# Kernel optimization log

Measured on AMD Instinct MI355X. Metric: run time of the kernel, lower is better.

## Reference

```python
import jax, jax.numpy as jnp
import numpy as np

HEAD_DIM = 64  # self.head_dim, used only as the attention scale
D_MODEL = 1024


def setup_inputs() -> dict:
    key = jax.random.key(0)
    ks = jax.random.split(key, 6)
    B, S_NEW, S_CACHE, D = 4, 2048, 6144, D_MODEL
    w_scale = 1.0 / np.sqrt(D)  # keep logits well-conditioned
    return {
        "hidden_states": jax.random.normal(ks[0], (B, S_NEW, D), dtype=jnp.float32),
        "cached_key": jax.random.normal(ks[1], (B, S_CACHE, D), dtype=jnp.float32),
        "cached_value": jax.random.normal(ks[2], (B, S_CACHE, D), dtype=jnp.float32),
        "Wq": jax.random.normal(ks[3], (D, D), dtype=jnp.float32) * w_scale,
        "bq": jnp.zeros((D,), dtype=jnp.float32),
        "Wk": jax.random.normal(ks[4], (D, D), dtype=jnp.float32) * w_scale,
        "bk": jnp.zeros((D,), dtype=jnp.float32),
        "Wv": jax.random.normal(ks[5], (D, D), dtype=jnp.float32) * w_scale,
        "bv": jnp.zeros((D,), dtype=jnp.float32),
    }


def reference(hidden_states, cached_key, cached_value, Wq, bq, Wk, bk, Wv, bv):
    # Cached-branch forward: project new K/V, append to cache, full attention.
    # torch.nn.Linear: x @ W.T + b
    q = jnp.einsum("bsd,ed->bse", hidden_states, Wq) + bq          # [B, Sq, D]
    new_k = jnp.einsum("bsd,ed->bse", hidden_states, Wk) + bk      # [B, Sq, D]
    new_v = jnp.einsum("bsd,ed->bse", hidden_states, Wv) + bv
    k = jnp.concatenate([cached_key, new_k], axis=1)               # [B, Skv, D]
    v = jnp.concatenate([cached_value, new_v], axis=1)
    scale = 1.0 / jnp.sqrt(jnp.asarray(HEAD_DIM, dtype=q.dtype))
    scores = jnp.einsum("bqd,bkd->bqk", q, k) * scale              # [B, Sq, Skv]
    probs = jax.nn.softmax(scores, axis=-1)
    out = jnp.einsum("bqk,bkd->bqd", probs, v)                     # [B, Sq, D]
    return out
```

## Files before the change

### kernel.cpp

```cpp
#include <hip/hip_runtime.h>
#include <stdint.h>


#define DM 1024
#define NB 4
#define SQN 2048
#define SCC 6144
#define SKV 8192
#define NSPLIT 2
#define KSP (SKV / NSPLIT)

typedef unsigned short u16;
typedef __attribute__((ext_vector_type(8))) short short8;
typedef __attribute__((ext_vector_type(4))) float f32x4;

__device__ __forceinline__ u16 f2bf(float x) {
  unsigned u = __builtin_bit_cast(unsigned, x);
  u += 0x7fffu + ((u >> 16) & 1u);
  return (u16)(u >> 16);
}

__device__ __forceinline__ void gll16(const void* g, void* l) {
  __builtin_amdgcn_global_load_lds(
      (const __attribute__((address_space(1))) void*)g,
      (__attribute__((address_space(3))) void*)l, 16, 0, 0);
}

#define FENCE() asm volatile("" ::: "memory")
#define BARRIER()                      \
  do {                                 \
    FENCE();                           \
    __builtin_amdgcn_s_barrier();      \
    FENCE();                           \
  } while (0)

__global__ __launch_bounds__(256) void k_cvt(const float* __restrict__ in,
                                             u16* __restrict__ out, long n4) {
  long i = (long)blockIdx.x * 256 + threadIdx.x;
  long st = (long)gridDim.x * 256;
  for (; i < n4; i += st) {
    float4 v = ((const float4*)in)[i];
    ushort4 u;
    u.x = f2bf(v.x); u.y = f2bf(v.y); u.z = f2bf(v.z); u.w = f2bf(v.w);
    ((ushort4*)out)[i] = u;
  }
}

__global__ __launch_bounds__(256) void k_cvt_ck(const float* __restrict__ in,
                                                u16* __restrict__ out) {
  const long n4 = (long)NB * SCC * DM / 4;
  long i = (long)blockIdx.x * 256 + threadIdx.x;
  long st = (long)gridDim.x * 256;
  for (; i < n4; i += st) {
    float4 v = ((const float4*)in)[i];
    ushort4 u;
    u.x = f2bf(v.x); u.y = f2bf(v.y); u.z = f2bf(v.z); u.w = f2bf(v.w);
    long e = i * 4;
    int b = (int)(e / ((long)SCC * DM));
    long rem = e - (long)b * SCC * DM;
    *(ushort4*)(out + (long)b * SKV * DM + rem) = u;
  }
}

__global__ __launch_bounds__(256) void k_build_vt(const float* __restrict__ cv,
                                                  const u16* __restrict__ vtmp,
                                                  u16* __restrict__ VT) {
  __shared__ u16 t[64][65];
  const int kv0 = blockIdx.x * 64;
  const int d0 = blockIdx.y * 64;
  const int b = blockIdx.z;
  const int c = threadIdx.x & 63;
  const int r4 = threadIdx.x >> 6;
#pragma unroll
  for (int p = 0; p < 16; ++p) {
    int kr = p * 4 + r4;
    int kv = kv0 + kr;
    int d = d0 + c;
    u16 u;
    if (kv < SCC)
      u = f2bf(cv[((long)b * SCC + kv) * DM + d]);
    else
      u = vtmp[((long)b * SQN + (kv - SCC)) * DM + d];
    t[kr][c] = u;
  }
  __syncthreads();
#pragma unroll
  for (int p = 0; p < 16; ++p) {
    int dr = p * 4 + r4;
    VT[((long)b * DM + d0 + dr) * SKV + kv0 + c] = t[c][dr];
  }
}

template <int MODE>
__global__ __launch_bounds__(512, 2) void k_gemm8(
    const u16* __restrict__ A, const u16* __restrict__ B0,
    void* __restrict__ C0, void* __restrict__ C1, void* __restrict__ C2,
    float* __restrict__ sums, const float* __restrict__ bias0,
    const float* __restrict__ bias1, const float* __restrict__ bias2) {
  extern __shared__ char smem[];
  const int tid = threadIdx.x;
  const int lane = tid & 63;
  const int wv = tid >> 6;
  const int wr = wv >> 2;
  const int wc = wv & 3;
  const int bm = blockIdx.y * 256;
  const int bn = blockIdx.x * 256;
  const int z = blockIdx.z;

  constexpr int LD = (MODE == 2) ? SKV : DM;
  constexpr int NT = ((MODE == 2) ? KSP : DM) / 64;

  const u16 *Ab, *Bb;
  if constexpr (MODE == 0) {
    Ab = A + (long)bm * LD;
    Bb = B0 + (long)bn * LD;
  } else if constexpr (MODE == 1) {
    Ab = A + ((long)z * SKV + bm) * LD;
    Bb = B0 + ((long)z * SQN + bn) * LD;
  } else {
    const int bb_ = z / NSPLIT, sp = z % NSPLIT;
    Ab = A + ((long)bb_ * SQN + bm) * (long)SKV + (long)sp * KSP;
    Bb = B0 + ((long)bb_ * DM + bn) * (long)SKV + (long)sp * KSP;
  }

  const int srow = wv * 8 + (lane >> 3);
  const int scol = ((lane & 7) ^ (lane >> 3)) * 8;
  const u16* gA = Ab + (long)srow * LD + scol;
  const u16* gB = Bb + (long)srow * LD + scol;
  u16* lA = (u16*)smem + wv * 512 + lane * 8;
  u16* lB = (u16*)(smem + 65536) + wv * 512 + lane * 8;

#pragma unroll
  for (int r = 0; r < 4; ++r) gll16(gA + (long)r * 64 * LD, lA + r * 4096);
#pragma unroll
  for (int r = 0; r < 4; ++r) gll16(gB + (long)r * 64 * LD, lB + r * 4096);

  f32x4 acc[8][4];
#pragma unroll
  for (int m = 0; m < 8; ++m)
#pragma unroll
    for (int n = 0; n < 4; ++n)
#pragma unroll
      for (int j = 0; j < 4; ++j) acc[m][n][j] = 0.0f;

  const int alane = lane & 15;
  const int sw = lane & 7;
  const int s0 = lane >> 4;

#define AFRAG(M, KK)                                                  \
  (*(const short8*)(As + (wr * 128 + (M)*16 + alane) * 128 +          \
                    (((s0 + 4 * (KK)) ^ sw) * 16)))
#define BFRAG(N, KK)                                                  \
  (*(const short8*)(Bs + (wc * 64 + (N)*16 + alane) * 128 +           \
                    (((s0 + 4 * (KK)) ^ sw) * 16)))
#define MFMA16(N0, N1)                                                      \
  __builtin_amdgcn_s_setprio(1);                                            \
  _Pragma("unroll") for (int m = 0; m < 8; ++m) {                           \
    acc[m][N0] = __builtin_amdgcn_mfma_f32_16x16x32_bf16(aF[m], bF[N0],     \
                                                         acc[m][N0], 0, 0, 0); \
    acc[m][N1] = __builtin_amdgcn_mfma_f32_16x16x32_bf16(aF[m], bF[N1],     \
                                                         acc[m][N1], 0, 0, 0); \
  }                                                                         \
  __builtin_amdgcn_s_setprio(0);

  short8 aF[8], bF[4];

  for (int kt = 0; kt < NT; ++kt) {
    const int b = kt & 1;
    const char* As = smem + b * 32768;
    const char* Bs = smem + 65536 + b * 32768;
    const int d = (b ^ 1) * 16384;
    const long knext = (long)((kt + 1 < NT) ? kt + 1 : kt) * 64;
    const u16* gAn = gA + knext;
    const u16* gBn = gB + knext;

    gll16(gAn, lA + d);
    gll16(gAn + (long)64 * LD, lA + d + 4096);
    asm volatile("s_waitcnt vmcnt(2)" ::: "memory");
    BARRIER();
#pragma unroll
    for (int m = 0; m < 8; ++m) aF[m] = AFRAG(m, 0);
#pragma unroll
    for (int n = 0; n < 4; ++n) bF[n] = BFRAG(n, 0);
    MFMA16(0, 1);
    BARRIER();

    gll16(gAn + (long)128 * LD, lA + d + 2 * 4096);
    gll16(gAn + (long)192 * LD, lA + d + 3 * 4096);
    BARRIER();
    MFMA16(2, 3);
    BARRIER();

#pragma unroll
    for (int m = 0; m < 8; ++m) aF[m] = AFRAG(m, 1);
#pragma unroll
    for (int n = 0; n < 4; ++n) bF[n] = BFRAG(n, 1);
    gll16(gBn, lB + d);
    gll16(gBn + (long)64 * LD, lB + d + 4096);
    BARRIER();
    MFMA16(0, 1);
    BARRIER();

    gll16(gBn + (long)128 * LD, lB + d + 2 * 4096);
    gll16(gBn + (long)192 * LD, lB + d + 3 * 4096);
    BARRIER();
    MFMA16(2, 3);
    BARRIER();
  }
#undef AFRAG
#undef BFRAG
#undef MFMA16

  const int rsub = (lane >> 4) * 4;

  if constexpr (MODE == 0) {
    const int which = bm >> 10;
    const float* bp = which == 0 ? bias0 : (which == 1 ? bias1 : bias2);
    u16* Cq = (u16*)C0;
    u16* Ck = (u16*)C1;
    u16* Cv = (u16*)C2;
    const int od_base = (bm & 1023) + wr * 128 + rsub;
#pragma unroll
    for (int n = 0; n < 4; ++n) {
      int token = bn + wc * 64 + n * 16 + alane;
      u16* dst;
      if (which == 1) {
        int b = token >> 11, ss = token & 2047;
        dst = Ck + ((long)b * SKV + SCC + ss) * DM;
      } else if (which == 0) {
        dst = Cq + (long)token * DM;
      } else {
        dst = Cv + (long)token * DM;
      }
#pragma unroll
      for (int m = 0; m < 8; ++m) {
        int cc = od_base + m * 16;
        float4 bb = *(const float4*)(bp + cc);
        ushort4 u;
        u.x = f2bf(acc[m][n][0] + bb.x);
        u.y = f2bf(acc[m][n][1] + bb.y);
        u.z = f2bf(acc[m][n][2] + bb.z);
        u.w = f2bf(acc[m][n][3] + bb.w);
        *(ushort4*)(dst + cc) = u;
      }
    }
  } else if constexpr (MODE == 1) {
    u16* Pp = (u16*)C0 + (long)z * SQN * SKV;
    float* sb = sums + z * SQN;
    const float CE = 0.18033688011112042f;
    const int kv_base = bm + wr * 128 + rsub;
#pragma unroll
    for (int n = 0; n < 4; ++n) {
      int q = bn + wc * 64 + n * 16 + alane;
      u16* prow = Pp + (long)q * SKV;
      float part = 0.f;
#pragma unroll
      for (int m = 0; m < 8; ++m) {
        int kv = kv_base + m * 16;
        float e0 = exp2f(acc[m][n][0] * CE);
        float e1 = exp2f(acc[m][n][1] * CE);
        float e2 = exp2f(acc[m][n][2] * CE);
        float e3 = exp2f(acc[m][n][3] * CE);
        part += (e0 + e1) + (e2 + e3);
        ushort4 u;
        u.x = f2bf(e0); u.y = f2bf(e1); u.z = f2bf(e2); u.w = f2bf(e3);
        *(ushort4*)(prow + kv) = u;
      }
      part += __shfl_xor(part, 16);
      part += __shfl_xor(part, 32);
      if ((lane >> 4) == 0) atomicAdd(&sb[q], part);
    }
  } else {
    float* Cp = (float*)C0 + (long)z * SQN * DM;
#pragma unroll
    for (int n = 0; n < 4; ++n) {
      int col = bn + wc * 64 + n * 16 + alane;
#pragma unroll
      for (int m = 0; m < 8; ++m)
#pragma unroll
        for (int j = 0; j < 4; ++j) {
          int row = bm + wr * 128 + m * 16 + rsub + j;
          Cp[(long)row * DM + col] = acc[m][n][j];
        }
    }
  }
}

__global__ __launch_bounds__(256) void k_reduce(const float* __restrict__ Op,
                                                const float* __restrict__ sums,
                                                float* __restrict__ out) {
  const long n4 = (long)NB * SQN * DM / 4;
  long i = (long)blockIdx.x * 256 + threadIdx.x;
  if (i >= n4) return;
  long e = i * 4;
  int b = (int)(e / ((long)SQN * DM));
  long rem = e - (long)b * SQN * DM;
  int row = (int)(rem / DM);
  const long z4 = (long)SQN * DM / 4;
  long i0 = (long)(b * NSPLIT) * z4 + (rem >> 2);
  float4 a0 = ((const float4*)Op)[i0];
  float4 a1 = ((const float4*)Op)[i0 + z4];
  float inv = 1.0f / sums[b * SQN + row];
  float4 r;
  r.x = (a0.x + a1.x) * inv;
  r.y = (a0.y + a1.y) * inv;
  r.z = (a0.z + a1.z) * inv;
  r.w = (a0.w + a1.w) * inv;
  ((float4*)out)[i] = r;
}

extern "C" void kernel_launch(void* const* d_in, const int* in_sizes, int n_in,
                              void* d_out, int out_size, void* d_ws, size_t ws_size,
                              hipStream_t stream) {
  const float* hidden = (const float*)d_in[0];
  const float* ck = (const float*)d_in[1];
  const float* cv = (const float*)d_in[2];
  const float* Wq = (const float*)d_in[3];
  const float* bq = (const float*)d_in[4];
  const float* Wk = (const float*)d_in[5];
  const float* bk = (const float*)d_in[6];
  const float* Wv = (const float*)d_in[7];
  const float* bv = (const float*)d_in[8];
  (void)in_sizes; (void)n_in; (void)out_size; (void)ws_size;

  hipFuncSetAttribute(reinterpret_cast<const void*>(&k_gemm8<0>),
                      hipFuncAttributeMaxDynamicSharedMemorySize, 131072);
  hipFuncSetAttribute(reinterpret_cast<const void*>(&k_gemm8<1>),
                      hipFuncAttributeMaxDynamicSharedMemorySize, 131072);
  hipFuncSetAttribute(reinterpret_cast<const void*>(&k_gemm8<2>),
                      hipFuncAttributeMaxDynamicSharedMemorySize, 131072);

  char* base = (char*)d_ws;
  size_t off = 0;
  auto alloc = [&](size_t bytes) {
    char* p = base + off;
    off = (off + bytes + 255) & ~(size_t)255;
    return p;
  };
  u16* Hb = (u16*)alloc((size_t)NB * SQN * DM * 2);
  u16* Wall = (u16*)alloc((size_t)3 * DM * DM * 2);
  u16* Qb = (u16*)alloc((size_t)NB * SQN * DM * 2);
  u16* Kb = (u16*)alloc((size_t)NB * SKV * DM * 2);
  u16* Vtmp = (u16*)alloc((size_t)NB * SQN * DM * 2);
  float* Opart = (float*)base;
  size_t opart_bytes = (size_t)NB * NSPLIT * SQN * DM * 4;
  if (off < opart_bytes) off = (opart_bytes + 255) & ~(size_t)255;
  u16* VT = (u16*)alloc((size_t)NB * DM * SKV * 2);
  u16* P = (u16*)alloc((size_t)NB * SQN * SKV * 2);
  float* sums = (float*)alloc((size_t)NB * SQN * 4);

  k_cvt<<<2048, 256, 0, stream>>>(hidden, Hb, (long)NB * SQN * DM / 4);
  k_cvt<<<512, 256, 0, stream>>>(Wq, Wall, (long)DM * DM / 4);
  k_cvt<<<512, 256, 0, stream>>>(Wk, Wall + (size_t)DM * DM, (long)DM * DM / 4);
  k_cvt<<<512, 256, 0, stream>>>(Wv, Wall + (size_t)2 * DM * DM, (long)DM * DM / 4);
  k_cvt_ck<<<4096, 256, 0, stream>>>(ck, Kb);

  k_gemm8<0><<<dim3(32, 12, 1), 512, 131072, stream>>>(
      Wall, Hb, Qb, Kb, Vtmp, nullptr, bq, bk, bv);

  k_build_vt<<<dim3(SKV / 64, DM / 64, NB), 256, 0, stream>>>(cv, Vtmp, VT);

  hipMemsetAsync(sums, 0, (size_t)NB * SQN * 4, stream);
  k_gemm8<1><<<dim3(SQN / 256, SKV / 256, NB), 512, 131072, stream>>>(
      Kb, Qb, P, nullptr, nullptr, sums, nullptr, nullptr, nullptr);

  k_gemm8<2><<<dim3(DM / 256, SQN / 256, NB * NSPLIT), 512, 131072, stream>>>(
      P, VT, Opart, nullptr, nullptr, nullptr, nullptr, nullptr, nullptr);

  k_reduce<<<(NB * SQN * DM / 4 + 255) / 256, 256, 0, stream>>>(
      Opart, sums, (float*)d_out);
}
```

Before: 475.9 us.

## Hand-schedule LDS fragment reads with inline asm and partial lgkmcnt waits

Replaces the compiler-generated LDS fragment loads in the GEMM main loop with explicit ds_read_b128 inline asm using immediate offsets. The MFMA work is regrouped into four 4x4 quadrants, and fine-grained lgkmcnt waits plus sched_barriers let LDS reads for later quadrants overlap with MFMAs on earlier ones. The goal is to hide LDS latency and reduce address arithmetic. The cost is more live fragment registers and fragile hand scheduling. The asm reads declare no memory clobber, which could let the compiler move them across barriers.

```diff
diff --git a/kernel.cpp b/kernel.cpp
--- a/kernel.cpp
+++ b/kernel.cpp
@@ -32,6 +32,26 @@
     FENCE();                           \
     __builtin_amdgcn_s_barrier();      \
     FENCE();                           \
+  } while (0)
+
+#define DSR(d, a, I) \
+  asm volatile("ds_read_b128 %0, %1 offset:" #I : "=v"(d) : "v"(a))
+
+#define LGKM(N)                                   \
+  do {                                            \
+    asm volatile("s_waitcnt lgkmcnt(" #N ")");    \
+    __builtin_amdgcn_sched_barrier(0);            \
+  } while (0)
+
+#define MFMAQ(AF, BF, MB)                                                   \
+  do {                                                                      \
+    __builtin_amdgcn_s_setprio(1);                                          \
+    _Pragma("unroll") for (int m = 0; m < 4; ++m)                           \
+        _Pragma("unroll") for (int n = 0; n < 4; ++n) acc[(MB) + m][n] =    \
+        __builtin_amdgcn_mfma_f32_16x16x32_bf16(AF[m], BF[n],               \
+                                                acc[(MB) + m][n], 0, 0, 0); \
+    __builtin_amdgcn_s_setprio(0);                                          \
+    __builtin_amdgcn_sched_barrier(0);                                      \
   } while (0)
 
 __global__ __launch_bounds__(256) void k_cvt(const float* __restrict__ in,
@@ -110,23 +130,23 @@
   constexpr int LD = (MODE == 2) ? SKV : DM;
   constexpr int NT = ((MODE == 2) ? KSP : DM) / 64;
 
-  const u16 *Ab, *Bb;
+  const u16 *Ab_, *Bb_;
   if constexpr (MODE == 0) {
-    Ab = A + (long)bm * LD;
-    Bb = B0 + (long)bn * LD;
+    Ab_ = A + (long)bm * LD;
+    Bb_ = B0 + (long)bn * LD;
   } else if constexpr (MODE == 1) {
-    Ab = A + ((long)z * SKV + bm) * LD;
-    Bb = B0 + ((long)z * SQN + bn) * LD;
+    Ab_ = A + ((long)z * SKV + bm) * LD;
+    Bb_ = B0 + ((long)z * SQN + bn) * LD;
   } else {
     const int bb_ = z / NSPLIT, sp = z % NSPLIT;
-    Ab = A + ((long)bb_ * SQN + bm) * (long)SKV + (long)sp * KSP;
-    Bb = B0 + ((long)bb_ * DM + bn) * (long)SKV + (long)sp * KSP;
+    Ab_ = A + ((long)bb_ * SQN + bm) * (long)SKV + (long)sp * KSP;
+    Bb_ = B0 + ((long)bb_ * DM + bn) * (long)SKV + (long)sp * KSP;
   }
 
   const int srow = wv * 8 + (lane >> 3);
   const int scol = ((lane & 7) ^ (lane >> 3)) * 8;
-  const u16* gA = Ab + (long)srow * LD + scol;
-  const u16* gB = Bb + (long)srow * LD + scol;
+  const u16* gA = Ab_ + (long)srow * LD + scol;
+  const u16* gB = Bb_ + (long)srow * LD + scol;
   u16* lA = (u16*)smem + wv * 512 + lane * 8;
   u16* lB = (u16*)(smem + 65536) + wv * 512 + lane * 8;
 
@@ -146,70 +166,65 @@
   const int alane = lane & 15;
   const int sw = lane & 7;
   const int s0 = lane >> 4;
-
-#define AFRAG(M, KK)                                                  \
-  (*(const short8*)(As + (wr * 128 + (M)*16 + alane) * 128 +          \
-                    (((s0 + 4 * (KK)) ^ sw) * 16)))
-#define BFRAG(N, KK)                                                  \
-  (*(const short8*)(Bs + (wc * 64 + (N)*16 + alane) * 128 +           \
-                    (((s0 + 4 * (KK)) ^ sw) * 16)))
-#define MFMA16(N0, N1)                                                      \
-  __builtin_amdgcn_s_setprio(1);                                            \
-  _Pragma("unroll") for (int m = 0; m < 8; ++m) {                           \
-    acc[m][N0] = __builtin_amdgcn_mfma_f32_16x16x32_bf16(aF[m], bF[N0],     \
-                                                         acc[m][N0], 0, 0, 0); \
-    acc[m][N1] = __builtin_amdgcn_mfma_f32_16x16x32_bf16(aF[m], bF[N1],     \
-                                                         acc[m][N1], 0, 0, 0); \
-  }                                                                         \
-  __builtin_amdgcn_s_setprio(0);
-
-  short8 aF[8], bF[4];
+  const int slot0 = ((s0 ^ sw) * 16);
+  const int slot1 = (((s0 + 4) ^ sw) * 16);
+  const int arow_b = (wr * 128 + alane) * 128;
+  const int brow_b = (wc * 64 + alane) * 128;
+
+  short8 Aa[4], Abf[4], Bf0[4], Bf1[4];
 
   for (int kt = 0; kt < NT; ++kt) {
-    const int b = kt & 1;
-    const char* As = smem + b * 32768;
-    const char* Bs = smem + 65536 + b * 32768;
-    const int d = (b ^ 1) * 16384;
+    const int bsel = (kt & 1) * 32768;
+    const int d = ((kt & 1) ^ 1) * 16384;
     const long knext = (long)((kt + 1 < NT) ? kt + 1 : kt) * 64;
     const u16* gAn = gA + knext;
     const u16* gBn = gB + knext;
+    const int a0 = bsel + arow_b + slot0;
+    const int a1 = bsel + arow_b + slot1;
+    const int b0 = 65536 + bsel + brow_b + slot0;
+    const int b1 = 65536 + bsel + brow_b + slot1;
 
     gll16(gAn, lA + d);
     gll16(gAn + (long)64 * LD, lA + d + 4096);
     asm volatile("s_waitcnt vmcnt(2)" ::: "memory");
     BARRIER();
-#pragma unroll
-    for (int m = 0; m < 8; ++m) aF[m] = AFRAG(m, 0);
-#pragma unroll
-    for (int n = 0; n < 4; ++n) bF[n] = BFRAG(n, 0);
-    MFMA16(0, 1);
-    BARRIER();
-
+    DSR(Aa[0], a0, 0); DSR(Aa[1], a0, 2048);
+    DSR(Aa[2], a0, 4096); DSR(Aa[3], a0, 6144);
+    DSR(Bf0[0], b0, 0); DSR(Bf0[1], b0, 2048);
+    DSR(Bf0[2], b0, 4096); DSR(Bf0[3], b0, 6144);
+    DSR(Abf[0], a0, 8192); DSR(Abf[1], a0, 10240);
+    DSR(Abf[2], a0, 12288); DSR(Abf[3], a0, 14336);
+    LGKM(4);
+    MFMAQ(Aa, Bf0, 0);
+    BARRIER();
+
+    DSR(Aa[0], a1, 0); DSR(Aa[1], a1, 2048);
+    DSR(Aa[2], a1, 4096); DSR(Aa[3], a1, 6144);
+    DSR(Bf1[0], b1, 0); DSR(Bf1[1], b1, 2048);
+    DSR(Bf1[2], b1, 4096); DSR(Bf1[3], b1, 6144);
     gll16(gAn + (long)128 * LD, lA + d + 2 * 4096);
     gll16(gAn + (long)192 * LD, lA + d + 3 * 4096);
     BARRIER();
-    MFMA16(2, 3);
-    BARRIER();
-
-#pragma unroll
-    for (int m = 0; m < 8; ++m) aF[m] = AFRAG(m, 1);
-#pragma unroll
-    for (int n = 0; n < 4; ++n) bF[n] = BFRAG(n, 1);
+    LGKM(8);
+    MFMAQ(Abf, Bf0, 4);
+    BARRIER();
+
+    DSR(Abf[0], a1, 8192); DSR(Abf[1], a1, 10240);
+    DSR(Abf[2], a1, 12288); DSR(Abf[3], a1, 14336);
     gll16(gBn, lB + d);
     gll16(gBn + (long)64 * LD, lB + d + 4096);
     BARRIER();
-    MFMA16(0, 1);
+    LGKM(4);
+    MFMAQ(Aa, Bf1, 0);
     BARRIER();
 
     gll16(gBn + (long)128 * LD, lB + d + 2 * 4096);
     gll16(gBn + (long)192 * LD, lB + d + 3 * 4096);
     BARRIER();
-    MFMA16(2, 3);
-    BARRIER();
-  }
-#undef AFRAG
-#undef BFRAG
-#undef MFMA16
+    LGKM(0);
+    MFMAQ(Abf, Bf1, 4);
+    BARRIER();
+  }
 
   const int rsub = (lane >> 4) * 4;
 
```

Result: no change. 471.3 us (-1.0%).
